# Performance work log

Hardware: AMD Instinct MI355X
Metric: run time of the kernel (lower is better)

Reference implementation:

```python
import jax, jax.numpy as jnp
import numpy as np

SCALE = 28.0
ALPHA = 0.6
BETA = 0.4
SCALE_POS = 10.0
SCALE_NEG = 40.0
NUM_CLASSES = 11003
FEATURE_SIZE = 2048
BATCH = 1024


def setup_inputs() -> dict:
    key = jax.random.key(0)
    k1, k2, k3, k4 = jax.random.split(key, 4)
    visual_embed = jax.random.normal(k1, (BATCH, FEATURE_SIZE), dtype=jnp.float32)
    textual_embed = jax.random.normal(k2, (BATCH, FEATURE_SIZE), dtype=jnp.float32)
    labels = jax.random.randint(k3, (BATCH,), 0, NUM_CLASSES, dtype=jnp.int64)
    W = jax.random.normal(k4, (FEATURE_SIZE, NUM_CLASSES), dtype=jnp.float32)
    return {"visual_embed": visual_embed, "textual_embed": textual_embed,
            "labels": labels, "W": W}


def _l2norm(x, axis):
    return x / jnp.linalg.norm(x, axis=axis, keepdims=True)


def _cross_entropy(logits, labels):
    logp = jax.nn.log_softmax(logits, axis=-1)
    return -jnp.take_along_axis(logp, labels[:, None], axis=-1).mean()


def reference(visual_embed, textual_embed, labels, W):
    b = visual_embed.shape[0]
    v = _l2norm(visual_embed, 1)
    t = _l2norm(textual_embed, 1)

    # instance loss: scaled cosine classifier + CE on both modalities
    Wn = _l2norm(W, 0)
    v_logits = SCALE * (v @ Wn)
    t_logits = SCALE * (t @ Wn)
    instance_loss = _cross_entropy(v_logits, labels) + _cross_entropy(t_logits, labels)

    # global align loss: masked soft-margin over full BxB similarity.
    # Original loops rows i and columns i, so every entry is counted twice.
    sim = v @ t.T  # [B, B]
    pos_mask = (labels[:, None] == labels[None, :]).astype(sim.dtype)
    loss_pos = jax.nn.softplus(-SCALE_POS * (sim - ALPHA))
    loss_neg = jax.nn.softplus(SCALE_NEG * (sim - BETA))
    per_pair = pos_mask * loss_pos + (1.0 - pos_mask) * loss_neg
    global_align_loss = 2.0 * per_pair.sum() / b

    return jnp.stack([instance_loss, global_align_loss])
```

## Files before the change

### kernel.cpp

```cpp
#include <hip/hip_runtime.h>
#include <hip/hip_bf16.h>
#include <math.h>

#define BATCH 1024
#define FEAT  2048
#define NCLS  11003
#define NPAD  11008
#define NT1   86
#define NPART (NT1 * 2)
#define M1    2048
#define C_SCALE  28.0f
#define C_ALPHA  0.6f
#define C_BETA   0.4f
#define C_SPOS   10.0f
#define C_SNEG   40.0f
#define XSCALE   16.0f
#define SCL1     (C_SCALE / XSCALE)
#define SIMSCL   (1.0f / (XSCALE * XSCALE))
#define SCALE1   0x7F7F7F7F

typedef float floatx4 __attribute__((ext_vector_type(4)));
typedef float f32x16  __attribute__((ext_vector_type(16)));
typedef int   v8i     __attribute__((ext_vector_type(8)));
typedef unsigned char u8;

#define O_ALIGN  ((size_t)0)
#define O_INST   ((size_t)64)
#define O_FIN    ((size_t)128)
#define O_COLSQ  ((size_t)256)
#define O_XN     ((size_t)44288)
#define O_WT     ((size_t)4238592)
#define O_PSUM   ((size_t)26782976)
#define O_LL     ((size_t)28192000)

#define PREP_WBLOCKS (43 * 32)
#define PREP_TOTAL   (PREP_WBLOCKS + M1)

__device__ inline float softplusf(float x) {
    return (x > 20.f) ? x : log1pf(expf(x));
}

__device__ inline void gll16(const void* g, void* l) {
    __builtin_amdgcn_global_load_lds(
        (const __attribute__((address_space(1))) unsigned int*)g,
        (__attribute__((address_space(3))) unsigned int*)l, 16, 0, 0);
}

__device__ inline unsigned int pack4_fp8(float a, float b, float c, float d) {
    unsigned int p = __builtin_amdgcn_cvt_pk_fp8_f32(a, b, 0, false);
    p = __builtin_amdgcn_cvt_pk_fp8_f32(c, d, p, true);
    return p;
}

__device__ inline int swz(int c) { return c ^ ((c >> 4) & 7); }

__global__ __launch_bounds__(256) void k_prep(const float* __restrict__ vis,
                                              const float* __restrict__ txt,
                                              const float* __restrict__ W,
                                              u8* __restrict__ Xn,
                                              u8* __restrict__ WT,
                                              float* __restrict__ colsq) {
    __shared__ u8 tileT[1024 * 16];
    __shared__ float cps[4][256];
    __shared__ float sb[256];
    int t = threadIdx.x;
    if (blockIdx.x < PREP_WBLOCKS) {
        int c0 = (blockIdx.x % 43) * 256, f0 = (blockIdx.x / 43) * 64;
        int w = t >> 6, l = t & 63;
        int cbase = c0 + 4 * l;
        unsigned int chunks[4][4];
        float ssq0 = 0.f, ssq1 = 0.f, ssq2 = 0.f, ssq3 = 0.f;
        #pragma unroll
        for (int q = 0; q < 4; ++q) {
            float4 row[4];
            #pragma unroll
            for (int rr = 0; rr < 4; ++rr) {
                int f = f0 + w * 16 + q * 4 + rr;
                const float* p = W + (size_t)f * NCLS + cbase;
                float4 v;
                if (cbase + 3 < NCLS) {
                    __builtin_memcpy(&v, p, 16);
                } else {
                    v.x = (cbase + 0 < NCLS) ? p[0] : 0.f;
                    v.y = (cbase + 1 < NCLS) ? p[1] : 0.f;
                    v.z = (cbase + 2 < NCLS) ? p[2] : 0.f;
                    v.w = (cbase + 3 < NCLS) ? p[3] : 0.f;
                }
                row[rr] = v;
            }
            chunks[0][q] = pack4_fp8(row[0].x, row[1].x, row[2].x, row[3].x);
            chunks[1][q] = pack4_fp8(row[0].y, row[1].y, row[2].y, row[3].y);
            chunks[2][q] = pack4_fp8(row[0].z, row[1].z, row[2].z, row[3].z);
            chunks[3][q] = pack4_fp8(row[0].w, row[1].w, row[2].w, row[3].w);
            #pragma unroll
            for (int rr = 0; rr < 4; ++rr) {
                ssq0 += row[rr].x * row[rr].x;
                ssq1 += row[rr].y * row[rr].y;
                ssq2 += row[rr].z * row[rr].z;
                ssq3 += row[rr].w * row[rr].w;
            }
        }
        #pragma unroll
        for (int j = 0; j < 4; ++j) {
            int L = (4 * l + j) * 4 + w;
            int P = L ^ ((L >> 4) & 7);
            *(uint4*)(tileT + P * 16) =
                make_uint4(chunks[j][0], chunks[j][1], chunks[j][2], chunks[j][3]);
        }
        *(float4*)&cps[w][4 * l] = make_float4(ssq0, ssq1, ssq2, ssq3);
        __syncthreads();
        int c = c0 + t;
        uint4 och[4];
        #pragma unroll
        for (int w2 = 0; w2 < 4; ++w2) {
            int L = t * 4 + w2;
            int P = L ^ ((L >> 4) & 7);
            och[w2] = *(const uint4*)(tileT + P * 16);
        }
        uint4* dst = (uint4*)(WT + (size_t)c * FEAT + f0);
        dst[0] = och[0]; dst[1] = och[1]; dst[2] = och[2]; dst[3] = och[3];
        float s = cps[0][t] + cps[1][t] + cps[2][t] + cps[3][t];
        if (c < NCLS) atomicAdd(&colsq[c], s);
    } else {
        int r = blockIdx.x - PREP_WBLOCKS;
        const float* src = (r < BATCH) ? (vis + (size_t)r * FEAT)
                                       : (txt + (size_t)(r - BATCH) * FEAT);
        float4 x0 = ((const float4*)src)[t];
        float4 x1 = ((const float4*)src)[t + 256];
        float ss = x0.x*x0.x + x0.y*x0.y + x0.z*x0.z + x0.w*x0.w
                 + x1.x*x1.x + x1.y*x1.y + x1.z*x1.z + x1.w*x1.w;
        sb[t] = ss; __syncthreads();
        for (int s = 128; s > 0; s >>= 1) { if (t < s) sb[t] += sb[t + s]; __syncthreads(); }
        float rn = rsqrtf(sb[0]) * XSCALE;
        unsigned int* dst = (unsigned int*)(Xn + (size_t)r * FEAT);
        dst[t]       = pack4_fp8(x0.x*rn, x0.y*rn, x0.z*rn, x0.w*rn);
        dst[t + 256] = pack4_fp8(x1.x*rn, x1.y*rn, x1.z*rn, x1.w*rn);
    }
}

__global__ __launch_bounds__(256) void k_gemm(const u8* __restrict__ Xn,
                                              const u8* __restrict__ WT,
                                              const float* __restrict__ colsq,
                                              const int* __restrict__ labels,
                                              float* __restrict__ psum,
                                              float* __restrict__ ll,
                                              float* __restrict__ align_sum) {
    __shared__ u8 As[128 * 64], Bs[128 * 64];
    f32x16 acc[2][2] = {};
    const int t = threadIdx.x;
    const bool is_sim = (blockIdx.y >= NT1);
    int m0, n0;
    const u8 *A, *B;
    if (!is_sim) {
        m0 = blockIdx.x * 128; n0 = blockIdx.y * 128;
        A = Xn; B = WT;
    } else {
        int s = (blockIdx.y - NT1) * 16 + blockIdx.x;
        m0 = (s >> 3) * 128; n0 = (s & 7) * 128;
        A = Xn; B = Xn + (size_t)BATCH * FEAT;
    }
    const int c0s = swz(t), c1s = swz(256 + t);
    const int ra0 = c0s >> 2, h0 = c0s & 3;
    const int ra1 = c1s >> 2, h1 = c1s & 3;
    const u8* Ag0 = A + (size_t)(m0 + ra0) * FEAT + h0 * 16;
    const u8* Ag1 = A + (size_t)(m0 + ra1) * FEAT + h1 * 16;
    const u8* Bg0 = B + (size_t)(n0 + ra0) * FEAT + h0 * 16;
    const u8* Bg1 = B + (size_t)(n0 + ra1) * FEAT + h1 * 16;
    u8* lA0 = As + t * 16;
    u8* lA1 = As + 4096 + t * 16;
    u8* lB0 = Bs + t * 16;
    u8* lB1 = Bs + 4096 + t * 16;

    const int wave = t >> 6, lane = t & 63;
    const int wm = wave >> 1, wn = wave & 1;
    const int l32 = lane & 31, kh = lane >> 5;
    const uint4* Ard[2][2]; const uint4* Brd[2][2];
    #pragma unroll
    for (int i = 0; i < 2; ++i) {
        #pragma unroll
        for (int c = 0; c < 2; ++c) {
            Ard[i][c] = (const uint4*)(As + swz((wm*64 + i*32 + l32)*4 + kh*2 + c) * 16);
            Brd[i][c] = (const uint4*)(Bs + swz((wn*64 + i*32 + l32)*4 + kh*2 + c) * 16);
        }
    }
    for (int kt = 0; kt < FEAT / 64; ++kt) {
        __syncthreads();
        gll16(Ag0, lA0);
        gll16(Ag1, lA1);
        gll16(Bg0, lB0);
        gll16(Bg1, lB1);
        Ag0 += 64; Ag1 += 64; Bg0 += 64; Bg1 += 64;
        __syncthreads();
        v8i a[2], b[2];
        #pragma unroll
        for (int i = 0; i < 2; ++i) {
            ((uint4*)&a[i])[0] = *Ard[i][0];
            ((uint4*)&a[i])[1] = *Ard[i][1];
            ((uint4*)&b[i])[0] = *Brd[i][0];
            ((uint4*)&b[i])[1] = *Brd[i][1];
        }
        #pragma unroll
        for (int i = 0; i < 2; ++i)
            #pragma unroll
            for (int j = 0; j < 2; ++j)
                acc[i][j] = __builtin_amdgcn_mfma_scale_f32_32x32x64_f8f6f4(
                    a[i], b[j], acc[i][j], 0, 0, 0, SCALE1, 0, SCALE1);
    }

    if (!is_sim) {
        float rcol[2]; bool val[2]; int ncol[2];
        #pragma unroll
        for (int j = 0; j < 2; ++j) {
            ncol[j] = n0 + wn*64 + j*32 + l32;
            val[j] = (ncol[j] < NCLS);
            rcol[j] = val[j] ? (SCL1 * rsqrtf(colsq[ncol[j]])) : 0.f;
        }
        const int pidx = blockIdx.y * 2 + wn;
        #pragma unroll
        for (int i = 0; i < 2; ++i) {
            #pragma unroll
            for (int reg = 0; reg < 16; ++reg) {
                int m = m0 + wm*64 + i*32 + (reg & 3) + 8*(reg >> 2) + 4*kh;
                int lm = labels[m & (BATCH - 1)];
                float s = 0.f;
                #pragma unroll
                for (int j = 0; j < 2; ++j) {
                    if (val[j]) {
                        float v = acc[i][j][reg] * rcol[j];
                        if (ncol[j] == lm) ll[m] = v;
                        s += __expf(v - C_SCALE);
                    }
                }
                #pragma unroll
                for (int off = 1; off < 32; off <<= 1) s += __shfl_xor(s, off);
                if (l32 == 0) psum[(size_t)m * NPART + pidx] = s;
            }
        }
    } else {
        int ln[2];
        #pragma unroll
        for (int j = 0; j < 2; ++j) ln[j] = labels[n0 + wn*64 + j*32 + l32];
        float tot = 0.f;
        #pragma unroll
        for (int i = 0; i < 2; ++i) {
            #pragma unroll
            for (int reg = 0; reg < 16; ++reg) {
                int m = m0 + wm*64 + i*32 + (reg & 3) + 8*(reg >> 2) + 4*kh;
                int lm = labels[m];
                #pragma unroll
                for (int j = 0; j < 2; ++j) {
                    float s = acc[i][j][reg] * SIMSCL;
                    float arg = (lm == ln[j]) ? (-C_SPOS * (s - C_ALPHA))
                                              : ( C_SNEG * (s - C_BETA));
                    tot += softplusf(arg);
                }
            }
        }
        #pragma unroll
        for (int off = 1; off < 64; off <<= 1) tot += __shfl_xor(tot, off);
        if (lane == 0) atomicAdd(align_sum, tot);
    }
}

__global__ __launch_bounds__(256) void k_merge(const float* __restrict__ psum,
                                               const float* __restrict__ ll,
                                               float* __restrict__ inst_sum,
                                               const float* __restrict__ align_sum,
                                               int* __restrict__ fin,
                                               float* __restrict__ out) {
    int r = blockIdx.x, t = threadIdx.x;
    float sm = (t < NPART) ? psum[(size_t)r * NPART + t] : 0.f;
    __shared__ float sb[256];
    sb[t] = sm; __syncthreads();
    for (int s = 128; s > 0; s >>= 1) { if (t < s) sb[t] += sb[t+s]; __syncthreads(); }
    if (t == 0) {
        atomicAdd(inst_sum, C_SCALE + logf(sb[0]) - ll[r]);
        __threadfence();
        if (atomicAdd(fin, 1) == M1 - 1) {
            __threadfence();
            float is = atomicAdd(inst_sum, 0.f);
            float as = atomicAdd((float*)align_sum, 0.f);
            out[0] = is / (float)BATCH;
            out[1] = as * 2.f / (float)BATCH;
        }
    }
}

extern "C" void kernel_launch(void* const* d_in, const int* in_sizes, int n_in,
                              void* d_out, int out_size, void* d_ws, size_t ws_size,
                              hipStream_t stream) {
    const float* vis    = (const float*)d_in[0];
    const float* txt    = (const float*)d_in[1];
    const int*   labels = (const int*)  d_in[2];
    const float* W      = (const float*)d_in[3];
    float* out = (float*)d_out;
    char*  ws  = (char*)d_ws;

    float* align_sum = (float*)(ws + O_ALIGN);
    float* inst_sum  = (float*)(ws + O_INST);
    int*   fin       = (int*)  (ws + O_FIN);
    float* colsq     = (float*)(ws + O_COLSQ);
    u8* Xn = (u8*)(ws + O_XN);
    u8* WT = (u8*)(ws + O_WT);
    float* psum = (float*)(ws + O_PSUM);
    float* ll   = (float*)(ws + O_LL);

    hipMemsetAsync(ws, 0, O_XN, stream);

    k_prep <<<dim3(PREP_TOTAL), 256, 0, stream>>>(vis, txt, W, Xn, WT, colsq);
    k_gemm <<<dim3(M1 / 128, NT1 + 4), 256, 0, stream>>>(Xn, WT, colsq, labels,
                                                         psum, ll, align_sum);
    k_merge<<<dim3(M1), 256, 0, stream>>>(psum, ll, inst_sum, align_sum, fin, out);
}
```

Before: 294.3 us.

## Fuse CE merge into GEMM via last-block reduction and double K-tile depth

Removes the separate merge kernel: each instance GEMM block increments a per-row-tile counter, and the last block to finish a row tile reduces the partial exp-sums (now stored transposed for coalesced reads) and adds to the loss. A global counter then finalizes outputs. The K step per LDS load is doubled from 64 to 128, halving barrier count at the cost of doubled LDS usage, which may reduce occupancy. The extra atomics and serialized tail reduction in the last blocks add some latency.

Result: slower. 330.8 us (+12.4%).

```diff
diff --git a/kernel.cpp b/kernel.cpp
--- a/kernel.cpp
+++ b/kernel.cpp
@@ -18,15 +18,16 @@
 #define SCL1     (C_SCALE / XSCALE)
 #define SIMSCL   (1.0f / (XSCALE * XSCALE))
 #define SCALE1   0x7F7F7F7F
-
-typedef float floatx4 __attribute__((ext_vector_type(4)));
-typedef float f32x16  __attribute__((ext_vector_type(16)));
-typedef int   v8i     __attribute__((ext_vector_type(8)));
+#define NFIN     80
+
+typedef float f32x16 __attribute__((ext_vector_type(16)));
+typedef int   v8i    __attribute__((ext_vector_type(8)));
 typedef unsigned char u8;
 
 #define O_ALIGN  ((size_t)0)
 #define O_INST   ((size_t)64)
 #define O_FIN    ((size_t)128)
+#define O_DONE   ((size_t)192)
 #define O_COLSQ  ((size_t)256)
 #define O_XN     ((size_t)44288)
 #define O_WT     ((size_t)4238592)
@@ -144,8 +145,14 @@
                                               const int* __restrict__ labels,
                                               float* __restrict__ psum,
                                               float* __restrict__ ll,
-                                              float* __restrict__ align_sum) {
-    __shared__ u8 As[128 * 64], Bs[128 * 64];
+                                              float* __restrict__ align_sum,
+                                              float* __restrict__ inst_sum,
+                                              int* __restrict__ fin,
+                                              int* __restrict__ done_m,
+                                              float* __restrict__ out) {
+    __shared__ u8 As[128 * 128], Bs[128 * 128];
+    __shared__ float sb[256];
+    __shared__ int last;
     f32x16 acc[2][2] = {};
     const int t = threadIdx.x;
     const bool is_sim = (blockIdx.y >= NT1);
@@ -159,52 +166,59 @@
         m0 = (s >> 3) * 128; n0 = (s & 7) * 128;
         A = Xn; B = Xn + (size_t)BATCH * FEAT;
     }
-    const int c0s = swz(t), c1s = swz(256 + t);
-    const int ra0 = c0s >> 2, h0 = c0s & 3;
-    const int ra1 = c1s >> 2, h1 = c1s & 3;
-    const u8* Ag0 = A + (size_t)(m0 + ra0) * FEAT + h0 * 16;
-    const u8* Ag1 = A + (size_t)(m0 + ra1) * FEAT + h1 * 16;
-    const u8* Bg0 = B + (size_t)(n0 + ra0) * FEAT + h0 * 16;
-    const u8* Bg1 = B + (size_t)(n0 + ra1) * FEAT + h1 * 16;
-    u8* lA0 = As + t * 16;
-    u8* lA1 = As + 4096 + t * 16;
-    u8* lB0 = Bs + t * 16;
-    u8* lB1 = Bs + 4096 + t * 16;
+    const u8* Ag[4]; const u8* Bg[4];
+    u8* lA[4]; u8* lB[4];
+    #pragma unroll
+    for (int s = 0; s < 4; ++s) {
+        int L = s * 256 + t;
+        int c = swz(L);
+        int row = c >> 3, h = c & 7;
+        Ag[s] = A + (size_t)(m0 + row) * FEAT + h * 16;
+        Bg[s] = B + (size_t)(n0 + row) * FEAT + h * 16;
+        lA[s] = As + L * 16;
+        lB[s] = Bs + L * 16;
+    }
 
     const int wave = t >> 6, lane = t & 63;
     const int wm = wave >> 1, wn = wave & 1;
     const int l32 = lane & 31, kh = lane >> 5;
-    const uint4* Ard[2][2]; const uint4* Brd[2][2];
+    const uint4* Ard[2][2][2]; const uint4* Brd[2][2][2];
     #pragma unroll
     for (int i = 0; i < 2; ++i) {
-        #pragma unroll
-        for (int c = 0; c < 2; ++c) {
-            Ard[i][c] = (const uint4*)(As + swz((wm*64 + i*32 + l32)*4 + kh*2 + c) * 16);
-            Brd[i][c] = (const uint4*)(Bs + swz((wn*64 + i*32 + l32)*4 + kh*2 + c) * 16);
-        }
-    }
-    for (int kt = 0; kt < FEAT / 64; ++kt) {
-        __syncthreads();
-        gll16(Ag0, lA0);
-        gll16(Ag1, lA1);
-        gll16(Bg0, lB0);
-        gll16(Bg1, lB1);
-        Ag0 += 64; Ag1 += 64; Bg0 += 64; Bg1 += 64;
-        __syncthreads();
-        v8i a[2], b[2];
-        #pragma unroll
-        for (int i = 0; i < 2; ++i) {
-            ((uint4*)&a[i])[0] = *Ard[i][0];
-            ((uint4*)&a[i])[1] = *Ard[i][1];
-            ((uint4*)&b[i])[0] = *Brd[i][0];
-            ((uint4*)&b[i])[1] = *Brd[i][1];
-        }
-        #pragma unroll
-        for (int i = 0; i < 2; ++i)
-            #pragma unroll
-            for (int j = 0; j < 2; ++j)
-                acc[i][j] = __builtin_amdgcn_mfma_scale_f32_32x32x64_f8f6f4(
-                    a[i], b[j], acc[i][j], 0, 0, 0, SCALE1, 0, SCALE1);
+        int rA = wm*64 + i*32 + l32;
+        int rB = wn*64 + i*32 + l32;
+        #pragma unroll
+        for (int ks = 0; ks < 2; ++ks)
+            #pragma unroll
+            for (int c = 0; c < 2; ++c) {
+                Ard[i][ks][c] = (const uint4*)(As + swz(rA*8 + ks*4 + kh*2 + c) * 16);
+                Brd[i][ks][c] = (const uint4*)(Bs + swz(rB*8 + ks*4 + kh*2 + c) * 16);
+            }
+    }
+    for (int kt = 0; kt < FEAT / 128; ++kt) {
+        __syncthreads();
+        #pragma unroll
+        for (int s = 0; s < 4; ++s) { gll16(Ag[s], lA[s]); gll16(Bg[s], lB[s]); }
+        #pragma unroll
+        for (int s = 0; s < 4; ++s) { Ag[s] += 128; Bg[s] += 128; }
+        __syncthreads();
+        #pragma unroll
+        for (int ks = 0; ks < 2; ++ks) {
+            v8i a[2], b[2];
+            #pragma unroll
+            for (int i = 0; i < 2; ++i) {
+                ((uint4*)&a[i])[0] = *Ard[i][ks][0];
+                ((uint4*)&a[i])[1] = *Ard[i][ks][1];
+                ((uint4*)&b[i])[0] = *Brd[i][ks][0];
+                ((uint4*)&b[i])[1] = *Brd[i][ks][1];
+            }
+            #pragma unroll
+            for (int i = 0; i < 2; ++i)
+                #pragma unroll
+                for (int j = 0; j < 2; ++j)
+                    acc[i][j] = __builtin_amdgcn_mfma_scale_f32_32x32x64_f8f6f4(
+                        a[i], b[j], acc[i][j], 0, 0, 0, SCALE1, 0, SCALE1);
+        }
     }
 
     if (!is_sim) {
@@ -233,7 +247,39 @@
                 }
                 #pragma unroll
                 for (int off = 1; off < 32; off <<= 1) s += __shfl_xor(s, off);
-                if (l32 == 0) psum[(size_t)m * NPART + pidx] = s;
+                if (l32 == 0) psum[(size_t)pidx * M1 + m] = s;
+            }
+        }
+        __syncthreads();
+        if (t == 0) {
+            __threadfence();
+            last = (atomicAdd(&done_m[blockIdx.x], 1) == NT1 - 1) ? 1 : 0;
+        }
+        __syncthreads();
+        if (last) {
+            __threadfence();
+            int ml = t & 127, half = t >> 7;
+            float s = 0.f;
+            for (int p = half; p < NPART; p += 2)
+                s += psum[(size_t)p * M1 + m0 + ml];
+            sb[t] = s; __syncthreads();
+            float ce = 0.f;
+            if (t < 128) ce = C_SCALE + logf(sb[t] + sb[t + 128]) - ll[m0 + t];
+            __syncthreads();
+            sb[t] = ce; __syncthreads();
+            for (int k2 = 128; k2 > 0; k2 >>= 1) {
+                if (t < k2) sb[t] += sb[t + k2];
+                __syncthreads();
+            }
+            if (t == 0) {
+                atomicAdd(inst_sum, sb[0]);
+                __threadfence();
+                if (atomicAdd(fin, 1) == NFIN - 1) {
+                    float is = atomicAdd(inst_sum, 0.f);
+                    float as = atomicAdd(align_sum, 0.f);
+                    out[0] = is / (float)BATCH;
+                    out[1] = as * 2.f / (float)BATCH;
+                }
             }
         }
     } else {
@@ -259,29 +305,15 @@
         #pragma unroll
         for (int off = 1; off < 64; off <<= 1) tot += __shfl_xor(tot, off);
         if (lane == 0) atomicAdd(align_sum, tot);
-    }
-}
-
-__global__ __launch_bounds__(256) void k_merge(const float* __restrict__ psum,
-                                               const float* __restrict__ ll,
-                                               float* __restrict__ inst_sum,
-                                               const float* __restrict__ align_sum,
-                                               int* __restrict__ fin,
-                                               float* __restrict__ out) {
-    int r = blockIdx.x, t = threadIdx.x;
-    float sm = (t < NPART) ? psum[(size_t)r * NPART + t] : 0.f;
-    __shared__ float sb[256];
-    sb[t] = sm; __syncthreads();
-    for (int s = 128; s > 0; s >>= 1) { if (t < s) sb[t] += sb[t+s]; __syncthreads(); }
-    if (t == 0) {
-        atomicAdd(inst_sum, C_SCALE + logf(sb[0]) - ll[r]);
-        __threadfence();
-        if (atomicAdd(fin, 1) == M1 - 1) {
+        __syncthreads();
+        if (t == 0) {
             __threadfence();
-            float is = atomicAdd(inst_sum, 0.f);
-            float as = atomicAdd((float*)align_sum, 0.f);
-            out[0] = is / (float)BATCH;
-            out[1] = as * 2.f / (float)BATCH;
+            if (atomicAdd(fin, 1) == NFIN - 1) {
+                float is = atomicAdd(inst_sum, 0.f);
+                float as = atomicAdd(align_sum, 0.f);
+                out[0] = is / (float)BATCH;
+                out[1] = as * 2.f / (float)BATCH;
+            }
         }
     }
 }
@@ -299,6 +331,7 @@
     float* align_sum = (float*)(ws + O_ALIGN);
     float* inst_sum  = (float*)(ws + O_INST);
     int*   fin       = (int*)  (ws + O_FIN);
+    int*   done_m    = (int*)  (ws + O_DONE);
     float* colsq     = (float*)(ws + O_COLSQ);
     u8* Xn = (u8*)(ws + O_XN);
     u8* WT = (u8*)(ws + O_WT);
@@ -307,8 +340,8 @@
 
     hipMemsetAsync(ws, 0, O_XN, stream);
 
-    k_prep <<<dim3(PREP_TOTAL), 256, 0, stream>>>(vis, txt, W, Xn, WT, colsq);
-    k_gemm <<<dim3(M1 / 128, NT1 + 4), 256, 0, stream>>>(Xn, WT, colsq, labels,
-                                                         psum, ll, align_sum);
-    k_merge<<<dim3(M1), 256, 0, stream>>>(psum, ll, inst_sum, align_sum, fin, out);
-}
+    k_prep<<<dim3(PREP_TOTAL), 256, 0, stream>>>(vis, txt, W, Xn, WT, colsq);
+    k_gemm<<<dim3(M1 / 128, NT1 + 4), 256, 0, stream>>>(Xn, WT, colsq, labels,
+                                                        psum, ll, align_sum,
+                                                        inst_sum, fin, done_m, out);
+}
```
